# Performance work log

Hardware: AMD Instinct MI355X
Metric: run time of the kernel (lower is better)

## Reference

```python
import jax, jax.numpy as jnp
import numpy as np

D = 512
B = 128
V = 1024
MAX_LEN = 5000


def _pos_encoding(d, max_len):
    # sinusoidal PE table [max_len, d], identical to the torch buffer
    pos = np.arange(max_len, dtype=np.float32)[:, None]
    div = np.exp(np.arange(0, d, 2, dtype=np.float32) * (-np.log(10000.0) / d))
    pe = np.zeros((max_len, d), dtype=np.float32)
    pe[:, 0::2] = np.sin(pos * div)
    pe[:, 1::2] = np.cos(pos * div)
    return jnp.asarray(pe)


def setup_inputs() -> dict:
    key = jax.random.key(0)
    ks = jax.random.split(key, 16)
    s = 0.02  # weight scale
    return {
        "x": jax.random.normal(ks[0], (B, V), jnp.float32),
        "timesteps": jax.random.randint(ks[1], (B,), 0, 1000),
        "query_emb": jax.random.normal(ks[2], (B, D), jnp.float32),
        "target_emb": jax.random.normal(ks[3], (B, V, D), jnp.float32),
        "Wq": jax.random.normal(ks[4], (D, D), jnp.float32) * s,
        "Wk": jax.random.normal(ks[5], (D, D), jnp.float32) * s,
        "Wv": jax.random.normal(ks[6], (D, D), jnp.float32) * s,
        "Wp": jax.random.normal(ks[7], (D, D), jnp.float32) * s,
        "bp": jnp.zeros((D,), jnp.float32),
        "Wt1": jax.random.normal(ks[8], (D, D), jnp.float32) * s,
        "bt1": jnp.zeros((D,), jnp.float32),
        "Wt2": jax.random.normal(ks[9], (D, D), jnp.float32) * s,
        "bt2": jnp.zeros((D,), jnp.float32),
        "Wd1": jax.random.normal(ks[10], (2 * D, 2 * D), jnp.float32) * s,
        "bd1": jnp.zeros((2 * D,), jnp.float32),
        "Wd2": jax.random.normal(ks[11], (1, 2 * D), jnp.float32) * s,
        "bd2": jnp.zeros((1,), jnp.float32),
    }


def reference(x, timesteps, query_emb, target_emb,
              Wq, Wk, Wv, Wp, bp, Wt1, bt1, Wt2, bt2,
              Wd1, bd1, Wd2, bd2):
    pe = _pos_encoding(D, MAX_LEN)
    # timestep embedding: pe[t] -> SiLU MLP  (dropout in eval mode = identity)
    t = pe[timesteps]                                      # [B, D]
    cond = jax.nn.silu(t @ Wt1.T + bt1) @ Wt2.T + bt2      # [B, D]
    q = (query_emb + cond) @ Wq.T                          # [B, D]
    tc = target_emb + cond[:, None, :]                     # [B, V, D]
    k = tc @ Wk.T
    v = tc @ Wv.T
    # single-query attention with additive bias x
    weight = jax.nn.softmax(jnp.einsum('bd,bvd->bv', q, k) + x, axis=-1)  # [B, V]
    new_emb = jnp.einsum('bv,bvd->bd', weight, v) @ Wp.T + bp             # [B, D]
    # concat-MLP decoder over all candidates
    emb = jnp.concatenate(
        [jnp.broadcast_to(new_emb[:, None, :], target_emb.shape), target_emb],
        axis=-1)                                            # [B, V, 2D]
    h = jax.nn.relu(emb @ Wd1.T + bd1)                      # [B, V, 2D]
    p = (h @ Wd2.T + bd2)[..., 0] + weight                  # [B, V]
    return p
```

## Files before the change

kernel.cpp:

```cpp
#include <hip/hip_runtime.h>
#include <hip/hip_bf16.h>


typedef __attribute__((ext_vector_type(8))) short bhalf8_t;
typedef __attribute__((ext_vector_type(8))) unsigned short ushort8_t;
typedef __attribute__((ext_vector_type(4))) float fx4_t;

__device__ __forceinline__ unsigned short f2bf(float f) {
  unsigned int u = __float_as_uint(f);
  unsigned int r = (u + 0x7FFFu + ((u >> 16) & 1u)) >> 16;
  return (unsigned short)r;
}
__device__ __forceinline__ float bf2f(unsigned short h) {
  return __uint_as_float((unsigned int)h << 16);
}

__device__ __forceinline__ float wave_sum64(float s) {
#pragma unroll
  for (int o = 32; o; o >>= 1) s += __shfl_xor(s, o, 64);
  return s;
}

__global__ __launch_bounds__(256) void prepw_kernel(
    const float* __restrict__ Wt1, const float* __restrict__ Wt2, const float* __restrict__ Wq,
    const float* __restrict__ Wv, const float* __restrict__ Wp, const float* __restrict__ Wd1,
    float* __restrict__ Wt1T, float* __restrict__ Wt2T, float* __restrict__ WqT,
    float* __restrict__ WvT, float* __restrict__ WpT, float* __restrict__ Wd1aT,
    unsigned short* __restrict__ wsW) {
  const int z = blockIdx.z;
  if (z == 6) {
    if (blockIdx.y >= 16) return;
    const int g = (blockIdx.y * 16 + blockIdx.x) * 256 + threadIdx.x;
    const int l = g & 63;
    const int u = g & 2047;
    const int stg = g >> 11;
    const int p = stg >> 4, ks = stg & 15;
    const int w = (u >> 8) & 7, n = (u >> 6) & 3;
    const int j = p * 512 + w * 64 + n * 16 + (l & 15);
    const int k = ks * 32 + (l >> 4) * 8;
    const float* src = Wd1 + (size_t)j * 1024 + 512 + k;
    float4 f0 = *(const float4*)src;
    float4 f1 = *(const float4*)(src + 4);
    ushort4 h0 = make_ushort4(f2bf(f0.x), f2bf(f0.y), f2bf(f0.z), f2bf(f0.w));
    ushort4 h1 = make_ushort4(f2bf(f1.x), f2bf(f1.y), f2bf(f1.z), f2bf(f1.w));
    ushort4* dst = (ushort4*)((char*)wsW + (size_t)g * 16);
    dst[0] = h0;
    dst[1] = h1;
    return;
  }
  __shared__ float t[32][33];
  const int tx = threadIdx.x & 31, ty = threadIdx.x >> 5;
  const int c0 = blockIdx.x * 32, r0 = blockIdx.y * 32;
  if (z == 5) {
    const float* src = Wd1;
    float* dst = Wd1aT;
#pragma unroll
    for (int i = 0; i < 32; i += 8)
      t[ty + i][tx] = src[(size_t)(r0 + ty + i) * 1024 + c0 + tx];
    __syncthreads();
#pragma unroll
    for (int i = 0; i < 32; i += 8)
      dst[(size_t)(c0 + ty + i) * 1024 + r0 + tx] = t[tx][ty + i];
    return;
  }
  if (blockIdx.y >= 16) return;
  const float* src;
  float* dst;
  switch (z) {
    case 0: src = Wt1; dst = Wt1T; break;
    case 1: src = Wt2; dst = Wt2T; break;
    case 2: src = Wq; dst = WqT; break;
    case 3: src = Wv; dst = WvT; break;
    default: src = Wp; dst = WpT; break;
  }
#pragma unroll
  for (int i = 0; i < 32; i += 8)
    t[ty + i][tx] = src[(size_t)(r0 + ty + i) * 512 + c0 + tx];
  __syncthreads();
#pragma unroll
  for (int i = 0; i < 32; i += 8)
    dst[(size_t)(c0 + ty + i) * 512 + r0 + tx] = t[tx][ty + i];
}

__global__ __launch_bounds__(512) void front_kernel(
    const int* __restrict__ timesteps, const float* __restrict__ qe,
    const float* __restrict__ Wt1T, const float* __restrict__ bt1,
    const float* __restrict__ Wt2T, const float* __restrict__ bt2,
    const float* __restrict__ WqT, const float* __restrict__ Wk,
    float* __restrict__ cond_out, float* __restrict__ qk_out, float* __restrict__ cb_out) {
  __shared__ __attribute__((aligned(16))) float v0[512], v1[512], v2[512];
  __shared__ float rd[8];
  const int b = blockIdx.x, tid = threadIdx.x;
  if (tid < 256) {
    const int ts = timesteps[b];
    const float NEG = -9.2103403719761836f / 512.f;
    float dv = expf((float)(2 * tid) * NEG);
    float ang = (float)ts * dv;
    v0[2 * tid] = sinf(ang);
    v0[2 * tid + 1] = cosf(ang);
  }
  __syncthreads();
  {
    float s0 = 0.f, s1 = 0.f, s2 = 0.f, s3 = 0.f;
#pragma unroll 4
    for (int k = 0; k < 512; k += 4) {
      s0 = fmaf(v0[k], Wt1T[(size_t)k * 512 + tid], s0);
      s1 = fmaf(v0[k + 1], Wt1T[(size_t)(k + 1) * 512 + tid], s1);
      s2 = fmaf(v0[k + 2], Wt1T[(size_t)(k + 2) * 512 + tid], s2);
      s3 = fmaf(v0[k + 3], Wt1T[(size_t)(k + 3) * 512 + tid], s3);
    }
    float s = (s0 + s1) + (s2 + s3) + bt1[tid];
    s = s / (1.f + expf(-s));
    v1[tid] = s;
  }
  __syncthreads();
  {
    float s0 = 0.f, s1 = 0.f, s2 = 0.f, s3 = 0.f;
#pragma unroll 4
    for (int k = 0; k < 512; k += 4) {
      s0 = fmaf(v1[k], Wt2T[(size_t)k * 512 + tid], s0);
      s1 = fmaf(v1[k + 1], Wt2T[(size_t)(k + 1) * 512 + tid], s1);
      s2 = fmaf(v1[k + 2], Wt2T[(size_t)(k + 2) * 512 + tid], s2);
      s3 = fmaf(v1[k + 3], Wt2T[(size_t)(k + 3) * 512 + tid], s3);
    }
    float s = (s0 + s1) + (s2 + s3) + bt2[tid];
    v0[tid] = s;
    cond_out[(size_t)b * 512 + tid] = s;
    v1[tid] = qe[(size_t)b * 512 + tid] + s;
  }
  __syncthreads();
  {
    float s0 = 0.f, s1 = 0.f, s2 = 0.f, s3 = 0.f;
#pragma unroll 4
    for (int k = 0; k < 512; k += 4) {
      s0 = fmaf(v1[k], WqT[(size_t)k * 512 + tid], s0);
      s1 = fmaf(v1[k + 1], WqT[(size_t)(k + 1) * 512 + tid], s1);
      s2 = fmaf(v1[k + 2], WqT[(size_t)(k + 2) * 512 + tid], s2);
      s3 = fmaf(v1[k + 3], WqT[(size_t)(k + 3) * 512 + tid], s3);
    }
    v2[tid] = (s0 + s1) + (s2 + s3);
  }
  __syncthreads();
  {
    float s0 = 0.f, s1 = 0.f, s2 = 0.f, s3 = 0.f;
#pragma unroll 4
    for (int d = 0; d < 512; d += 4) {
      s0 = fmaf(v2[d], Wk[(size_t)d * 512 + tid], s0);
      s1 = fmaf(v2[d + 1], Wk[(size_t)(d + 1) * 512 + tid], s1);
      s2 = fmaf(v2[d + 2], Wk[(size_t)(d + 2) * 512 + tid], s2);
      s3 = fmaf(v2[d + 3], Wk[(size_t)(d + 3) * 512 + tid], s3);
    }
    float qkv = (s0 + s1) + (s2 + s3);
    qk_out[(size_t)b * 512 + tid] = qkv;
    float p = wave_sum64(qkv * v0[tid]);
    if ((tid & 63) == 0) rd[tid >> 6] = p;
  }
  __syncthreads();
  if (tid == 0) {
    float c = 0.f;
#pragma unroll
    for (int w = 0; w < 8; ++w) c += rd[w];
    cb_out[b] = c;
  }
}

__global__ __launch_bounds__(512) void back_kernel(
    const float* __restrict__ spart, const float* __restrict__ cond,
    const float* __restrict__ WvT, const float* __restrict__ WpT, const float* __restrict__ bp,
    const float* __restrict__ Wd1aT, const float* __restrict__ bd1, float* __restrict__ Abuf) {
  __shared__ __attribute__((aligned(16))) float v0[512], v1[512];
  const int b = blockIdx.x, tid = threadIdx.x;
  {
    float s = cond[(size_t)b * 512 + tid];
#pragma unroll
    for (int q = 0; q < 8; ++q) s += spart[((size_t)b * 8 + q) * 512 + tid];
    v0[tid] = s;
  }
  __syncthreads();
  {
    float s0 = 0.f, s1 = 0.f, s2 = 0.f, s3 = 0.f;
#pragma unroll 4
    for (int k = 0; k < 512; k += 4) {
      s0 = fmaf(v0[k], WvT[(size_t)k * 512 + tid], s0);
      s1 = fmaf(v0[k + 1], WvT[(size_t)(k + 1) * 512 + tid], s1);
      s2 = fmaf(v0[k + 2], WvT[(size_t)(k + 2) * 512 + tid], s2);
      s3 = fmaf(v0[k + 3], WvT[(size_t)(k + 3) * 512 + tid], s3);
    }
    v1[tid] = (s0 + s1) + (s2 + s3);
  }
  __syncthreads();
  {
    float s0 = 0.f, s1 = 0.f, s2 = 0.f, s3 = 0.f;
#pragma unroll 4
    for (int k = 0; k < 512; k += 4) {
      s0 = fmaf(v1[k], WpT[(size_t)k * 512 + tid], s0);
      s1 = fmaf(v1[k + 1], WpT[(size_t)(k + 1) * 512 + tid], s1);
      s2 = fmaf(v1[k + 2], WpT[(size_t)(k + 2) * 512 + tid], s2);
      s3 = fmaf(v1[k + 3], WpT[(size_t)(k + 3) * 512 + tid], s3);
    }
    v0[tid] = (s0 + s1) + (s2 + s3) + bp[tid];
  }
  __syncthreads();
  {
    float a0 = 0.f, a1 = 0.f, b0 = 0.f, b1 = 0.f;
#pragma unroll 2
    for (int k = 0; k < 512; k += 2) {
      float x0 = v0[k], x1 = v0[k + 1];
      a0 = fmaf(x0, Wd1aT[(size_t)k * 1024 + tid], a0);
      a1 = fmaf(x1, Wd1aT[(size_t)(k + 1) * 1024 + tid], a1);
      b0 = fmaf(x0, Wd1aT[(size_t)k * 1024 + 512 + tid], b0);
      b1 = fmaf(x1, Wd1aT[(size_t)(k + 1) * 1024 + 512 + tid], b1);
    }
    Abuf[(size_t)b * 1024 + tid] = a0 + a1 + bd1[tid];
    Abuf[(size_t)b * 1024 + 512 + tid] = b0 + b1 + bd1[512 + tid];
  }
}

__global__ __launch_bounds__(256) void logits_kernel(
    const float* __restrict__ te, const float* __restrict__ qk,
    const float* __restrict__ constb, const float* __restrict__ x,
    float* __restrict__ logits, unsigned short* __restrict__ te16, int w16) {
  const int wave = threadIdx.x >> 6, lane = threadIdx.x & 63;
  const size_t r = (size_t)blockIdx.x * 4 + wave;
  const int b = (int)(r >> 10);
  const float4* t4 = (const float4*)(te + r * 512);
  const float4* q4 = (const float4*)(qk + (size_t)b * 512);
  float4 a0 = t4[lane], a1 = t4[lane + 64];
  float4 c0 = q4[lane], c1 = q4[lane + 64];
  float s = a0.x * c0.x + a0.y * c0.y + a0.z * c0.z + a0.w * c0.w +
            a1.x * c1.x + a1.y * c1.y + a1.z * c1.z + a1.w * c1.w;
  s = wave_sum64(s);
  if (w16) {
    ushort4 h0 = make_ushort4(f2bf(a0.x), f2bf(a0.y), f2bf(a0.z), f2bf(a0.w));
    ushort4 h1 = make_ushort4(f2bf(a1.x), f2bf(a1.y), f2bf(a1.z), f2bf(a1.w));
    *(ushort4*)(te16 + r * 512 + lane * 4) = h0;
    *(ushort4*)(te16 + r * 512 + 256 + lane * 4) = h1;
  }
  if (lane == 0) logits[r] = s + constb[b] + x[r];
}

__global__ __launch_bounds__(256) void softmax_kernel(
    const float* __restrict__ logits, const float* __restrict__ bd2,
    float* __restrict__ weight, float* __restrict__ out) {
  __shared__ float sm[4];
  const int b = blockIdx.x, tid = threadIdx.x;
  const int wave = tid >> 6, lane = tid & 63;
  float4 l4 = ((const float4*)(logits + (size_t)b * 1024))[tid];
  float m = fmaxf(fmaxf(l4.x, l4.y), fmaxf(l4.z, l4.w));
#pragma unroll
  for (int o = 32; o; o >>= 1) m = fmaxf(m, __shfl_xor(m, o, 64));
  if (lane == 0) sm[wave] = m;
  __syncthreads();
  float M = fmaxf(fmaxf(sm[0], sm[1]), fmaxf(sm[2], sm[3]));
  __syncthreads();
  float e0 = expf(l4.x - M), e1 = expf(l4.y - M), e2 = expf(l4.z - M), e3 = expf(l4.w - M);
  float ssum = wave_sum64(e0 + e1 + e2 + e3);
  if (lane == 0) sm[wave] = ssum;
  __syncthreads();
  float inv = 1.f / (sm[0] + sm[1] + sm[2] + sm[3]);
  float c = bd2[0];
  float4 w4 = make_float4(e0 * inv, e1 * inv, e2 * inv, e3 * inv);
  ((float4*)(weight + (size_t)b * 1024))[tid] = w4;
  ((float4*)(out + (size_t)b * 1024))[tid] = make_float4(w4.x + c, w4.y + c, w4.z + c, w4.w + c);
}

__global__ __launch_bounds__(256) void wsum32_kernel(const float* __restrict__ te,
                                                     const float* __restrict__ weight,
                                                     float* __restrict__ spart) {
  __shared__ float wl[128];
  const int b = blockIdx.x >> 3, vq = blockIdx.x & 7;
  const int tid = threadIdx.x;
  if (tid < 128) wl[tid] = weight[(size_t)b * 1024 + vq * 128 + tid];
  __syncthreads();
  const float* tb = te + ((size_t)b * 1024 + (size_t)vq * 128) * 512;
  float s0 = 0.f, s1 = 0.f;
#pragma unroll 4
  for (int v = 0; v < 128; ++v) {
    float w = wl[v];
    s0 += w * tb[(size_t)v * 512 + tid];
    s1 += w * tb[(size_t)v * 512 + 256 + tid];
  }
  spart[(size_t)blockIdx.x * 512 + tid] = s0;
  spart[(size_t)blockIdx.x * 512 + 256 + tid] = s1;
}

__global__ __launch_bounds__(256) void wsum16_kernel(const unsigned short* __restrict__ te16,
                                                     const float* __restrict__ weight,
                                                     float* __restrict__ spart) {
  __shared__ float wl[128];
  __shared__ float red[4][512];
  const int b = blockIdx.x >> 3, vq = blockIdx.x & 7;
  const int tid = threadIdx.x;
  if (tid < 128) wl[tid] = weight[(size_t)b * 1024 + vq * 128 + tid];
  __syncthreads();
  const int g = tid & 63, vh = tid >> 6;
  const unsigned short* base =
      te16 + ((size_t)b * 1024 + vq * 128 + vh * 32) * 512 + g * 8;
  float acc[8] = {};
  for (int v = 0; v < 32; ++v) {
    float w = wl[vh * 32 + v];
    ushort8_t h = *(const ushort8_t*)(base + (size_t)v * 512);
#pragma unroll
    for (int i = 0; i < 8; ++i) acc[i] += w * bf2f(h[i]);
  }
#pragma unroll
  for (int i = 0; i < 8; ++i) red[vh][g * 8 + i] = acc[i];
  __syncthreads();
  for (int d = tid; d < 512; d += 256)
    spart[(size_t)blockIdx.x * 512 + d] =
        red[0][d] + red[1][d] + red[2][d] + red[3][d];
}

#define GLD16(g, l)                                                              \
  __builtin_amdgcn_global_load_lds((const __attribute__((address_space(1))) void*)(g), \
                                   (__attribute__((address_space(3))) void*)(l), 16, 0, 0)

template <int USE16>
__global__ __launch_bounds__(512, 2) void decoder_kernel(
    const float* __restrict__ te, const unsigned short* __restrict__ te16,
    const unsigned short* __restrict__ wsW, const float* __restrict__ A,
    const float* __restrict__ Wd2, float* __restrict__ out) {
  extern __shared__ char lds[];
  char* ring = lds + 65536;

  const int tid = threadIdx.x;
  const int wave = tid >> 6, lane = tid & 63;
  const int lhi = lane >> 4, llo = lane & 15;
  const size_t row0 = (size_t)blockIdx.x * 64;
  const int b = (int)(blockIdx.x >> 4);

  float av[2][4], wv[2][4];
  {
    const float* A_g = A + (size_t)b * 1024;
#pragma unroll
    for (int p = 0; p < 2; ++p)
#pragma unroll
      for (int n = 0; n < 4; ++n) {
        const int j = p * 512 + wave * 64 + n * 16 + llo;
        av[p][n] = A_g[j];
        wv[p][n] = Wd2[j];
      }
  }
#pragma unroll
  for (int p = 0; p < 2; ++p)
#pragma unroll
    for (int n = 0; n < 4; ++n) asm volatile("" : "+v"(av[p][n]), "+v"(wv[p][n]));

  if (USE16) {
    const char* base = (const char*)te16 + row0 * 1024;
#pragma unroll
    for (int i = 0; i < 8; ++i) {
      const int f = wave * 8 + i;
      const int m = f & 3, s = f >> 2;
      GLD16(base + (size_t)(m * 16 + llo) * 1024 + s * 64 + lhi * 16, lds + f * 1024);
    }
  } else {
    const float* src = te + row0 * 512;
#pragma unroll
    for (int it = 0; it < 8; ++it) {
      int u = it * 512 + tid;
      int f = u >> 6, l = u & 63;
      int m = f & 3, s = f >> 2;
      int row = m * 16 + (l & 15);
      int col = s * 32 + (l >> 4) * 8;
      const float4* sp = (const float4*)(src + (size_t)row * 512 + col);
      float4 f0 = sp[0], f1 = sp[1];
      ushort4 h0 = make_ushort4(f2bf(f0.x), f2bf(f0.y), f2bf(f0.z), f2bf(f0.w));
      ushort4 h1 = make_ushort4(f2bf(f1.x), f2bf(f1.y), f2bf(f1.z), f2bf(f1.w));
      char* d = lds + f * 1024 + l * 16;
      *(ushort4*)d = h0;
      *(ushort4*)(d + 8) = h1;
    }
    asm volatile("s_waitcnt vmcnt(0) lgkmcnt(0)" ::: "memory");
  }

  auto stage = [&](int s) {
    const char* src = (const char*)wsW + (size_t)s * 32768 + wave * 1024 + lane * 16;
    char* dst = ring + (s % 3) * 32768 + wave * 1024;
    GLD16(src, dst);
    GLD16(src + 8192, dst + 8192);
    GLD16(src + 16384, dst + 16384);
    GLD16(src + 24576, dst + 24576);
  };
  stage(0);
  stage(1);

  const char* afrag = lds + lane * 16;
  fx4_t acc[4][4];
  const fx4_t zf = {0.f, 0.f, 0.f, 0.f};
  float pacc[4][4] = {};

#pragma unroll
  for (int p = 0; p < 2; ++p) {
#pragma unroll
    for (int m = 0; m < 4; ++m)
#pragma unroll
      for (int n = 0; n < 4; ++n) acc[m][n] = zf;
#pragma unroll
    for (int s = 0; s < 16; ++s) {
      const int g = p * 16 + s;
      if (g <= 30) asm volatile("s_waitcnt vmcnt(4)" ::: "memory");
      else         asm volatile("s_waitcnt vmcnt(0)" ::: "memory");
      __builtin_amdgcn_s_barrier();
      __builtin_amdgcn_sched_barrier(0);
      if (g <= 29) stage(g + 2);
      const char* wb = ring + (g % 3) * 32768 + wave * 4096 + lane * 16;
      bhalf8_t a0 = *(const bhalf8_t*)(afrag + (s * 4 + 0) * 1024);
      bhalf8_t a1 = *(const bhalf8_t*)(afrag + (s * 4 + 1) * 1024);
      bhalf8_t a2 = *(const bhalf8_t*)(afrag + (s * 4 + 2) * 1024);
      bhalf8_t a3 = *(const bhalf8_t*)(afrag + (s * 4 + 3) * 1024);
      bhalf8_t b0 = *(const bhalf8_t*)(wb);
      bhalf8_t b1 = *(const bhalf8_t*)(wb + 1024);
      bhalf8_t b2 = *(const bhalf8_t*)(wb + 2048);
      bhalf8_t b3 = *(const bhalf8_t*)(wb + 3072);
#pragma unroll
      for (int m = 0; m < 4; ++m) {
        bhalf8_t am = (m == 0) ? a0 : (m == 1) ? a1 : (m == 2) ? a2 : a3;
        acc[m][0] = __builtin_amdgcn_mfma_f32_16x16x32_bf16(am, b0, acc[m][0], 0, 0, 0);
        acc[m][1] = __builtin_amdgcn_mfma_f32_16x16x32_bf16(am, b1, acc[m][1], 0, 0, 0);
        acc[m][2] = __builtin_amdgcn_mfma_f32_16x16x32_bf16(am, b2, acc[m][2], 0, 0, 0);
        acc[m][3] = __builtin_amdgcn_mfma_f32_16x16x32_bf16(am, b3, acc[m][3], 0, 0, 0);
      }
      if (s == 15) {
#pragma unroll
        for (int n = 0; n < 4; ++n)
#pragma unroll
          for (int m = 0; m < 4; ++m)
#pragma unroll
            for (int rg = 0; rg < 4; ++rg)
              pacc[m][rg] += fmaxf(acc[m][n][rg] + av[p][n], 0.f) * wv[p][n];
      }
    }
  }

  float* red = (float*)ring;
#pragma unroll
  for (int m = 0; m < 4; ++m)
#pragma unroll
    for (int rg = 0; rg < 4; ++rg) {
      float sv = pacc[m][rg];
      sv += __shfl_xor(sv, 1, 64);
      sv += __shfl_xor(sv, 2, 64);
      sv += __shfl_xor(sv, 4, 64);
      sv += __shfl_xor(sv, 8, 64);
      if (llo == 0) red[wave * 64 + m * 16 + lhi * 4 + rg] = sv;
    }
  __syncthreads();
  if (tid < 64) {
    float s = 0.f;
#pragma unroll
    for (int w = 0; w < 8; ++w) s += red[w * 64 + tid];
    out[row0 + tid] += s;
  }
}

extern "C" void kernel_launch(void* const* d_in, const int* in_sizes, int n_in,
                              void* d_out, int out_size, void* d_ws, size_t ws_size,
                              hipStream_t stream) {
  const float* x = (const float*)d_in[0];
  const int* tsteps = (const int*)d_in[1];
  const float* qe = (const float*)d_in[2];
  const float* te = (const float*)d_in[3];
  const float* Wq = (const float*)d_in[4];
  const float* Wk = (const float*)d_in[5];
  const float* Wv = (const float*)d_in[6];
  const float* Wp = (const float*)d_in[7];
  const float* bp = (const float*)d_in[8];
  const float* Wt1 = (const float*)d_in[9];
  const float* bt1 = (const float*)d_in[10];
  const float* Wt2 = (const float*)d_in[11];
  const float* bt2 = (const float*)d_in[12];
  const float* Wd1 = (const float*)d_in[13];
  const float* bd1 = (const float*)d_in[14];
  const float* Wd2 = (const float*)d_in[15];
  const float* bd2 = (const float*)d_in[16];
  float* out = (float*)d_out;

  char* ws = (char*)d_ws;
  unsigned short* wsW = (unsigned short*)(ws + 0);
  float* Wt1T = (float*)(ws + 1048576);
  float* Wt2T = (float*)(ws + 2097152);
  float* WqT = (float*)(ws + 3145728);
  float* WvT = (float*)(ws + 4194304);
  float* WpT = (float*)(ws + 5242880);
  float* Wd1aT = (float*)(ws + 6291456);
  float* cond = (float*)(ws + 8388608);
  float* qk = (float*)(ws + 8650752);
  float* cb = (float*)(ws + 9961472);
  float* logits = (float*)(ws + 9965568);
  float* wgt = (float*)(ws + 10489856);
  float* spart = (float*)(ws + 11014144);
  float* Abuf = (float*)(ws + 13111296);
  const size_t TE16_OFF = 14680064;
  const size_t TE16_BYTES = (size_t)128 * 1024 * 512 * 2;
  unsigned short* te16 = (unsigned short*)(ws + TE16_OFF);
  const int use16 = (ws_size >= TE16_OFF + TE16_BYTES) ? 1 : 0;

  prepw_kernel<<<dim3(16, 32, 7), 256, 0, stream>>>(Wt1, Wt2, Wq, Wv, Wp, Wd1,
                                                    Wt1T, Wt2T, WqT, WvT, WpT, Wd1aT, wsW);
  front_kernel<<<128, 512, 0, stream>>>(tsteps, qe, Wt1T, bt1, Wt2T, bt2, WqT, Wk,
                                        cond, qk, cb);
  logits_kernel<<<32768, 256, 0, stream>>>(te, qk, cb, x, logits, te16, use16);
  softmax_kernel<<<128, 256, 0, stream>>>(logits, bd2, wgt, out);
  if (use16)
    wsum16_kernel<<<1024, 256, 0, stream>>>(te16, wgt, spart);
  else
    wsum32_kernel<<<1024, 256, 0, stream>>>(te, wgt, spart);
  back_kernel<<<128, 512, 0, stream>>>(spart, cond, WvT, WpT, bp, Wd1aT, bd1, Abuf);
  if (use16) {
    (void)hipFuncSetAttribute((const void*)decoder_kernel<1>,
                              hipFuncAttributeMaxDynamicSharedMemorySize, 163840);
    decoder_kernel<1><<<2048, 512, 163840, stream>>>(te, te16, wsW, Abuf, Wd2, out);
  } else {
    (void)hipFuncSetAttribute((const void*)decoder_kernel<0>,
                              hipFuncAttributeMaxDynamicSharedMemorySize, 163840);
    decoder_kernel<0><<<2048, 512, 163840, stream>>>(te, te16, wsW, Abuf, Wd2, out);
  }
}
```

Baseline: 414.4 us.

## Fuse softmax, weighted sum and back MLP into one per-batch tail kernel

```diff
diff --git a/kernel.cpp b/kernel.cpp
--- a/kernel.cpp
+++ b/kernel.cpp
@@ -164,16 +164,113 @@
   }
 }
 
-__global__ __launch_bounds__(512) void back_kernel(
-    const float* __restrict__ spart, const float* __restrict__ cond,
-    const float* __restrict__ WvT, const float* __restrict__ WpT, const float* __restrict__ bp,
-    const float* __restrict__ Wd1aT, const float* __restrict__ bd1, float* __restrict__ Abuf) {
+__global__ __launch_bounds__(256) void logits_kernel(
+    const float* __restrict__ te, const float* __restrict__ qk,
+    const float* __restrict__ constb, const float* __restrict__ x,
+    float* __restrict__ logits, unsigned short* __restrict__ te16, int w16) {
+  const int wave = threadIdx.x >> 6, lane = threadIdx.x & 63;
+  const size_t base = (size_t)blockIdx.x * 64;
+  const int b = (int)(base >> 10);
+  const float4* q4 = (const float4*)(qk + (size_t)b * 512);
+  const float4 c0 = q4[lane], c1 = q4[lane + 64];
+  const float cbv = constb[b];
+#pragma unroll 2
+  for (int i = 0; i < 16; ++i) {
+    const size_t r = base + (size_t)i * 4 + wave;
+    const float4* t4 = (const float4*)(te + r * 512);
+    float4 a0 = t4[lane], a1 = t4[lane + 64];
+    float s = a0.x * c0.x + a0.y * c0.y + a0.z * c0.z + a0.w * c0.w +
+              a1.x * c1.x + a1.y * c1.y + a1.z * c1.z + a1.w * c1.w;
+    s = wave_sum64(s);
+    if (w16) {
+      ushort4 h0 = make_ushort4(f2bf(a0.x), f2bf(a0.y), f2bf(a0.z), f2bf(a0.w));
+      ushort4 h1 = make_ushort4(f2bf(a1.x), f2bf(a1.y), f2bf(a1.z), f2bf(a1.w));
+      *(ushort4*)(te16 + r * 512 + lane * 4) = h0;
+      *(ushort4*)(te16 + r * 512 + 256 + lane * 4) = h1;
+    }
+    if (lane == 0) logits[r] = s + cbv + x[r];
+  }
+}
+
+template <int USE16>
+__global__ __launch_bounds__(512) void tail_kernel(
+    const float* __restrict__ te, const unsigned short* __restrict__ te16,
+    const float* __restrict__ logits, const float* __restrict__ bd2,
+    const float* __restrict__ cond, const float* __restrict__ WvT,
+    const float* __restrict__ WpT, const float* __restrict__ bp,
+    const float* __restrict__ Wd1aT, const float* __restrict__ bd1,
+    float* __restrict__ Abuf, float* __restrict__ out) {
+  __shared__ float wlds[1024];
+  __shared__ float red[8][512];
   __shared__ __attribute__((aligned(16))) float v0[512], v1[512];
+  __shared__ float rd[8];
+  __shared__ float sm[2];
   const int b = blockIdx.x, tid = threadIdx.x;
+  const int wave = tid >> 6, lane = tid & 63;
+
+  const float l0 = logits[(size_t)b * 1024 + tid];
+  const float l1 = logits[(size_t)b * 1024 + 512 + tid];
+  float m = fmaxf(l0, l1);
+#pragma unroll
+  for (int o = 32; o; o >>= 1) m = fmaxf(m, __shfl_xor(m, o, 64));
+  if (lane == 0) rd[wave] = m;
+  __syncthreads();
+  if (tid == 0) {
+    float M = rd[0];
+#pragma unroll
+    for (int w = 1; w < 8; ++w) M = fmaxf(M, rd[w]);
+    sm[0] = M;
+  }
+  __syncthreads();
+  const float M = sm[0];
+  const float e0 = expf(l0 - M), e1 = expf(l1 - M);
+  float ss = wave_sum64(e0 + e1);
+  if (lane == 0) rd[wave] = ss;
+  __syncthreads();
+  if (tid == 0) {
+    float S = 0.f;
+#pragma unroll
+    for (int w = 0; w < 8; ++w) S += rd[w];
+    sm[1] = 1.f / S;
+  }
+  __syncthreads();
+  const float inv = sm[1];
+  const float w0 = e0 * inv, w1 = e1 * inv;
+  wlds[tid] = w0;
+  wlds[tid + 512] = w1;
+  const float c = bd2[0];
+  out[(size_t)b * 1024 + tid] = w0 + c;
+  out[(size_t)b * 1024 + 512 + tid] = w1 + c;
+  __syncthreads();
+
+  const int g = tid & 63, vh = tid >> 6;
+  float acc[8] = {};
+  if (USE16) {
+    const unsigned short* base = te16 + ((size_t)b * 1024 + vh * 128) * 512 + g * 8;
+    for (int v = 0; v < 128; ++v) {
+      float w = wlds[vh * 128 + v];
+      ushort8_t h = *(const ushort8_t*)(base + (size_t)v * 512);
+#pragma unroll
+      for (int i = 0; i < 8; ++i) acc[i] += w * bf2f(h[i]);
+    }
+  } else {
+    const float* base = te + ((size_t)b * 1024 + vh * 128) * 512 + g * 8;
+    for (int v = 0; v < 128; ++v) {
+      float w = wlds[vh * 128 + v];
+      float4 f0 = *(const float4*)(base + (size_t)v * 512);
+      float4 f1 = *(const float4*)(base + (size_t)v * 512 + 4);
+      acc[0] += w * f0.x; acc[1] += w * f0.y; acc[2] += w * f0.z; acc[3] += w * f0.w;
+      acc[4] += w * f1.x; acc[5] += w * f1.y; acc[6] += w * f1.z; acc[7] += w * f1.w;
+    }
+  }
+#pragma unroll
+  for (int i = 0; i < 8; ++i) red[vh][g * 8 + i] = acc[i];
+  __syncthreads();
+
   {
     float s = cond[(size_t)b * 512 + tid];
 #pragma unroll
-    for (int q = 0; q < 8; ++q) s += spart[((size_t)b * 8 + q) * 512 + tid];
+    for (int h = 0; h < 8; ++h) s += red[h][tid];
     v0[tid] = s;
   }
   __syncthreads();
@@ -214,101 +311,6 @@
     Abuf[(size_t)b * 1024 + tid] = a0 + a1 + bd1[tid];
     Abuf[(size_t)b * 1024 + 512 + tid] = b0 + b1 + bd1[512 + tid];
   }
-}
-
-__global__ __launch_bounds__(256) void logits_kernel(
-    const float* __restrict__ te, const float* __restrict__ qk,
-    const float* __restrict__ constb, const float* __restrict__ x,
-    float* __restrict__ logits, unsigned short* __restrict__ te16, int w16) {
-  const int wave = threadIdx.x >> 6, lane = threadIdx.x & 63;
-  const size_t r = (size_t)blockIdx.x * 4 + wave;
-  const int b = (int)(r >> 10);
-  const float4* t4 = (const float4*)(te + r * 512);
-  const float4* q4 = (const float4*)(qk + (size_t)b * 512);
-  float4 a0 = t4[lane], a1 = t4[lane + 64];
-  float4 c0 = q4[lane], c1 = q4[lane + 64];
-  float s = a0.x * c0.x + a0.y * c0.y + a0.z * c0.z + a0.w * c0.w +
-            a1.x * c1.x + a1.y * c1.y + a1.z * c1.z + a1.w * c1.w;
-  s = wave_sum64(s);
-  if (w16) {
-    ushort4 h0 = make_ushort4(f2bf(a0.x), f2bf(a0.y), f2bf(a0.z), f2bf(a0.w));
-    ushort4 h1 = make_ushort4(f2bf(a1.x), f2bf(a1.y), f2bf(a1.z), f2bf(a1.w));
-    *(ushort4*)(te16 + r * 512 + lane * 4) = h0;
-    *(ushort4*)(te16 + r * 512 + 256 + lane * 4) = h1;
-  }
-  if (lane == 0) logits[r] = s + constb[b] + x[r];
-}
-
-__global__ __launch_bounds__(256) void softmax_kernel(
-    const float* __restrict__ logits, const float* __restrict__ bd2,
-    float* __restrict__ weight, float* __restrict__ out) {
-  __shared__ float sm[4];
-  const int b = blockIdx.x, tid = threadIdx.x;
-  const int wave = tid >> 6, lane = tid & 63;
-  float4 l4 = ((const float4*)(logits + (size_t)b * 1024))[tid];
-  float m = fmaxf(fmaxf(l4.x, l4.y), fmaxf(l4.z, l4.w));
-#pragma unroll
-  for (int o = 32; o; o >>= 1) m = fmaxf(m, __shfl_xor(m, o, 64));
-  if (lane == 0) sm[wave] = m;
-  __syncthreads();
-  float M = fmaxf(fmaxf(sm[0], sm[1]), fmaxf(sm[2], sm[3]));
-  __syncthreads();
-  float e0 = expf(l4.x - M), e1 = expf(l4.y - M), e2 = expf(l4.z - M), e3 = expf(l4.w - M);
-  float ssum = wave_sum64(e0 + e1 + e2 + e3);
-  if (lane == 0) sm[wave] = ssum;
-  __syncthreads();
-  float inv = 1.f / (sm[0] + sm[1] + sm[2] + sm[3]);
-  float c = bd2[0];
-  float4 w4 = make_float4(e0 * inv, e1 * inv, e2 * inv, e3 * inv);
-  ((float4*)(weight + (size_t)b * 1024))[tid] = w4;
-  ((float4*)(out + (size_t)b * 1024))[tid] = make_float4(w4.x + c, w4.y + c, w4.z + c, w4.w + c);
-}
-
-__global__ __launch_bounds__(256) void wsum32_kernel(const float* __restrict__ te,
-                                                     const float* __restrict__ weight,
-                                                     float* __restrict__ spart) {
-  __shared__ float wl[128];
-  const int b = blockIdx.x >> 3, vq = blockIdx.x & 7;
-  const int tid = threadIdx.x;
-  if (tid < 128) wl[tid] = weight[(size_t)b * 1024 + vq * 128 + tid];
-  __syncthreads();
-  const float* tb = te + ((size_t)b * 1024 + (size_t)vq * 128) * 512;
-  float s0 = 0.f, s1 = 0.f;
-#pragma unroll 4
-  for (int v = 0; v < 128; ++v) {
-    float w = wl[v];
-    s0 += w * tb[(size_t)v * 512 + tid];
-    s1 += w * tb[(size_t)v * 512 + 256 + tid];
-  }
-  spart[(size_t)blockIdx.x * 512 + tid] = s0;
-  spart[(size_t)blockIdx.x * 512 + 256 + tid] = s1;
-}
-
-__global__ __launch_bounds__(256) void wsum16_kernel(const unsigned short* __restrict__ te16,
-                                                     const float* __restrict__ weight,
-                                                     float* __restrict__ spart) {
-  __shared__ float wl[128];
-  __shared__ float red[4][512];
-  const int b = blockIdx.x >> 3, vq = blockIdx.x & 7;
-  const int tid = threadIdx.x;
-  if (tid < 128) wl[tid] = weight[(size_t)b * 1024 + vq * 128 + tid];
-  __syncthreads();
-  const int g = tid & 63, vh = tid >> 6;
-  const unsigned short* base =
-      te16 + ((size_t)b * 1024 + vq * 128 + vh * 32) * 512 + g * 8;
-  float acc[8] = {};
-  for (int v = 0; v < 32; ++v) {
-    float w = wl[vh * 32 + v];
-    ushort8_t h = *(const ushort8_t*)(base + (size_t)v * 512);
-#pragma unroll
-    for (int i = 0; i < 8; ++i) acc[i] += w * bf2f(h[i]);
-  }
-#pragma unroll
-  for (int i = 0; i < 8; ++i) red[vh][g * 8 + i] = acc[i];
-  __syncthreads();
-  for (int d = tid; d < 512; d += 256)
-    spart[(size_t)blockIdx.x * 512 + d] =
-        red[0][d] + red[1][d] + red[2][d] + red[3][d];
 }
 
 #define GLD16(g, l)                                                              \
@@ -488,8 +490,6 @@
   float* qk = (float*)(ws + 8650752);
   float* cb = (float*)(ws + 9961472);
   float* logits = (float*)(ws + 9965568);
-  float* wgt = (float*)(ws + 10489856);
-  float* spart = (float*)(ws + 11014144);
   float* Abuf = (float*)(ws + 13111296);
   const size_t TE16_OFF = 14680064;
   const size_t TE16_BYTES = (size_t)128 * 1024 * 512 * 2;
@@ -500,13 +500,13 @@
                                                     Wt1T, Wt2T, WqT, WvT, WpT, Wd1aT, wsW);
   front_kernel<<<128, 512, 0, stream>>>(tsteps, qe, Wt1T, bt1, Wt2T, bt2, WqT, Wk,
                                         cond, qk, cb);
-  logits_kernel<<<32768, 256, 0, stream>>>(te, qk, cb, x, logits, te16, use16);
-  softmax_kernel<<<128, 256, 0, stream>>>(logits, bd2, wgt, out);
+  logits_kernel<<<2048, 256, 0, stream>>>(te, qk, cb, x, logits, te16, use16);
   if (use16)
-    wsum16_kernel<<<1024, 256, 0, stream>>>(te16, wgt, spart);
+    tail_kernel<1><<<128, 512, 0, stream>>>(te, te16, logits, bd2, cond, WvT, WpT, bp,
+                                            Wd1aT, bd1, Abuf, out);
   else
-    wsum32_kernel<<<1024, 256, 0, stream>>>(te, wgt, spart);
-  back_kernel<<<128, 512, 0, stream>>>(spart, cond, WvT, WpT, bp, Wd1aT, bd1, Abuf);
+    tail_kernel<0><<<128, 512, 0, stream>>>(te, te16, logits, bd2, cond, WvT, WpT, bp,
+                                            Wd1aT, bd1, Abuf, out);
   if (use16) {
     (void)hipFuncSetAttribute((const void*)decoder_kernel<1>,
                               hipFuncAttributeMaxDynamicSharedMemorySize, 163840);
```

New measurement: 420.8 us. No clear change (+1.5%).
